# Kernel tuning notes

Measured on AMD Instinct MI355X. Metric: run time of the kernel, lower is better.

The kernel has to match this reference:

```python
import jax, jax.numpy as jnp
import numpy as np

H = 768       # hidden size
NH = 12       # num attention heads
DH = H // NH  # head dim = 64
B = 32
S = 512


def setup_inputs() -> dict:
    key = jax.random.key(0)
    ks = jax.random.split(key, 7)
    scale = 1.0 / np.sqrt(H)
    return {
        "inputs": jax.random.normal(ks[0], (B, S, H), dtype=jnp.float32),
        "Wq": jax.random.normal(ks[1], (H, H), dtype=jnp.float32) * scale,
        "bq": jnp.zeros((H,), dtype=jnp.float32),
        "Wk": jax.random.normal(ks[2], (H, H), dtype=jnp.float32) * scale,
        "bk": jnp.zeros((H,), dtype=jnp.float32),
        "Wv": jax.random.normal(ks[3], (H, H), dtype=jnp.float32) * scale,
        "bv": jnp.zeros((H,), dtype=jnp.float32),
    }


def reference(inputs, Wq, bq, Wk, bk, Wv, bv):
    # BertSelfAttention: linear projections (torch Linear: x @ W.T + b)
    def split_heads(x):  # [B,S,H] -> [B,NH,S,DH]
        return x.reshape(B, S, NH, DH).transpose(0, 2, 1, 3)

    q = split_heads(inputs @ Wq.T + bq)
    k = split_heads(inputs @ Wk.T + bk)
    v = split_heads(inputs @ Wv.T + bv)

    # scores [B,NH,S,S]; the wrapper adds an all-zero attention mask (no-op)
    scores = jnp.einsum("bhqd,bhkd->bhqk", q, k) / jnp.sqrt(jnp.float32(DH))
    probs = jax.nn.softmax(scores, axis=-1)
    ctx = jnp.einsum("bhqk,bhkd->bhqd", probs, v)  # [B,NH,S,DH]
    ctx = ctx.transpose(0, 2, 1, 3).reshape(B, S, H)
    return jnp.tanh(ctx)
```

## Files before the change

kernel.cpp:

```cpp
#include <hip/hip_runtime.h>
#include <hip/hip_bf16.h>
#include <cmath>

#define Bc   32
#define Sc_  512
#define Hc   768
#define NHc  12
#define DHc  64
#define Mc   (Bc * Sc_)
#define Ntot (3 * Hc)

#define QSCALE 0.18033688011112042f

typedef __attribute__((ext_vector_type(8))) short short8v;
typedef __attribute__((ext_vector_type(8))) unsigned short ushort8v;
typedef __attribute__((ext_vector_type(4))) float f32x4;

static __device__ __forceinline__ ushort f2b(float f) {
    __hip_bfloat16 h = __float2bfloat16(f);
    return *reinterpret_cast<ushort*>(&h);
}
static __device__ __forceinline__ ushort2 f2b2(float a, float b) {
    __hip_bfloat162 h = __float22bfloat162_rn(float2{a, b});
    return *reinterpret_cast<ushort2*>(&h);
}

static __device__ __forceinline__ void gl2lds(const ushort* g, ushort* l) {
    __builtin_amdgcn_global_load_lds(
        (const __attribute__((address_space(1))) unsigned int*)g,
        (__attribute__((address_space(3))) unsigned int*)l, 16, 0, 0);
}

static __device__ __forceinline__ float fast_tanh(float x) {
    float e = __builtin_amdgcn_exp2f(x * 2.885390081777927f);
    return 1.0f - 2.0f * __builtin_amdgcn_rcpf(e + 1.0f);
}

__global__ __launch_bounds__(256) void convert_pack(
    const float* __restrict__ X,
    const float* __restrict__ Wq, const float* __restrict__ Wk,
    const float* __restrict__ Wv,
    const float* __restrict__ bq, const float* __restrict__ bk,
    const float* __restrict__ bv,
    ushort* __restrict__ Xt, ushort* __restrict__ Wt, float* __restrict__ bbp)
{
    const int bx = blockIdx.x;
    const int panel = bx / 12, kcg = bx % 12;
    const int t = threadIdx.x;

    __shared__ ushort T[128][68];

    const float* base;
    ushort* out;
    if (panel < 128) {
        base = X + (size_t)panel * 128 * Hc;
        out  = Xt + (size_t)panel * (96 * 1024);
    } else {
        int nblk = panel - 128;
        int n0 = nblk * 128;
        int z = n0 / Hc;
        int nn0 = n0 - z * Hc;
        const float* W = (z == 0) ? Wq : (z == 1) ? Wk : Wv;
        base = W + (size_t)nn0 * Hc;
        out  = Wt + (size_t)nblk * (96 * 1024);
    }
    const int k0 = kcg * 64;

    const int slot = t & 15, rsub = t >> 4;
    #pragma unroll
    for (int rnd = 0; rnd < 8; ++rnd) {
        int row = rnd * 16 + rsub;
        const float* p = base + (size_t)row * Hc + k0 + slot * 4;
        float4 f = *(const float4*)p;
        ushort2 h0 = f2b2(f.x, f.y);
        ushort2 h1 = f2b2(f.z, f.w);
        ushort4 u;
        u.x = h0.x; u.y = h0.y; u.z = h1.x; u.w = h1.y;
        *(ushort4*)&T[row][slot * 4] = u;
    }
    __syncthreads();

    const int row_w = t & 127, kh = t >> 7;
    #pragma unroll
    for (int rnd = 0; rnd < 4; ++rnd) {
        int kc_l = rnd * 2 + kh;
        ushort4 lo = *(const ushort4*)&T[row_w][kc_l * 8];
        ushort4 hi = *(const ushort4*)&T[row_w][kc_l * 8 + 4];
        ushort8v o;
        o[0] = lo.x; o[1] = lo.y; o[2] = lo.z; o[3] = lo.w;
        o[4] = hi.x; o[5] = hi.y; o[6] = hi.z; o[7] = hi.w;
        *(ushort8v*)&out[(size_t)(kcg * 8 + kc_l) * 1024 + row_w * 8] = o;
    }

    if (bx == 0) {
        for (int i = t; i < Ntot; i += 256) {
            int z = i / Hc, nn = i - z * Hc;
            bbp[i] = ((z == 0) ? bq : (z == 1) ? bk : bv)[nn];
        }
    }
}

__global__ __launch_bounds__(256) void qkv_mfma(
    const ushort* __restrict__ Xt, const ushort* __restrict__ Wt,
    const float* __restrict__ bbp,
    ushort* __restrict__ Qb, ushort* __restrict__ Kt, ushort* __restrict__ Vt)
{
    const int tid = threadIdx.x;
    const int wave = tid >> 6, lane = tid & 63;
    const int quad = lane >> 4, l16 = lane & 15;
    const int wr = wave >> 1, wc = wave & 1;
    const int m0 = blockIdx.x * 128;
    const int n0 = blockIdx.y * 128;

    __shared__ __align__(16) ushort As[4096];
    __shared__ __align__(16) ushort Bs[4096];

    f32x4 acc[4][4];
    #pragma unroll
    for (int i = 0; i < 4; ++i)
        #pragma unroll
        for (int j = 0; j < 4; ++j) acc[i][j] = (f32x4)(0.f);

    const ushort* gA = Xt + (size_t)blockIdx.x * (96 * 1024) + wave * 1024 + lane * 8;
    const ushort* gB = Wt + (size_t)blockIdx.y * (96 * 1024) + wave * 1024 + lane * 8;
    ushort* lA = As + wave * 1024;
    ushort* lB = Bs + wave * 1024;

    for (int t = 0; t < 24; ++t) {
        const ushort* ga = gA + t * 4096;
        const ushort* gb = gB + t * 4096;
        gl2lds(ga,       lA);
        gl2lds(ga + 512, lA + 512);
        gl2lds(gb,       lB);
        gl2lds(gb + 512, lB + 512);
        __syncthreads();

        short8v a[4], b[4];
        #pragma unroll
        for (int i = 0; i < 4; ++i)
            a[i] = *(const short8v*)&As[quad * 1024 + (wr * 64 + i * 16 + l16) * 8];
        #pragma unroll
        for (int j = 0; j < 4; ++j)
            b[j] = *(const short8v*)&Bs[quad * 1024 + (wc * 64 + j * 16 + l16) * 8];
        #pragma unroll
        for (int i = 0; i < 4; ++i)
            #pragma unroll
            for (int j = 0; j < 4; ++j)
                acc[i][j] = __builtin_amdgcn_mfma_f32_16x16x32_bf16(
                    a[i], b[j], acc[i][j], 0, 0, 0);
        __syncthreads();
    }

    const int z = n0 / Hc;
    #pragma unroll
    for (int j = 0; j < 4; ++j) {
        const int n  = n0 + wc * 64 + j * 16 + l16;
        const int nn = n - z * Hc;
        const int h  = nn >> 6, d = nn & 63;
        const float bias = bbp[n];
        #pragma unroll
        for (int i = 0; i < 4; ++i) {
            const int mbase = m0 + wr * 64 + i * 16 + quad * 4;
            const int bb = mbase >> 9;
            const int s0 = mbase & 511;
            const size_t head = (size_t)(bb * NHc + h) * (Sc_ * DHc);
            if (z == 0) {
                size_t base = head + (size_t)s0 * DHc + d;
                #pragma unroll
                for (int r = 0; r < 4; ++r)
                    Qb[base + (size_t)r * DHc] = f2b((acc[i][j][r] + bias) * QSCALE);
            } else if (z == 1) {
                size_t base = head + (s0 >> 6) * 4096 + (d >> 3) * 512
                            + (s0 & 63) * 8 + (d & 7);
                #pragma unroll
                for (int r = 0; r < 4; ++r)
                    Kt[base + r * 8] = f2b(acc[i][j][r] + bias);
            } else {
                size_t base = head + (s0 >> 6) * 4096 + ((s0 & 63) >> 3) * 512
                            + d * 8 + (s0 & 7);
                ushort4 o;
                o.x = f2b(acc[i][j][0] + bias);
                o.y = f2b(acc[i][j][1] + bias);
                o.z = f2b(acc[i][j][2] + bias);
                o.w = f2b(acc[i][j][3] + bias);
                *(ushort4*)&Vt[base] = o;
            }
        }
    }
}

__global__ __launch_bounds__(256) void attn_mfma(
    const ushort* __restrict__ Qb, const ushort* __restrict__ Kt,
    const ushort* __restrict__ Vt, float* __restrict__ out)
{
    const int bid = blockIdx.x;
    const int super = bid >> 5, l = bid & 31;
    const int head_lin = super * 8 + (l & 7);
    const int qt = l >> 3;
    const int b = head_lin / NHc, h = head_lin % NHc;

    const int wave = threadIdx.x >> 6;
    const int lane = threadIdx.x & 63;
    const int quad = lane >> 4, l16 = lane & 15;
    const int q0 = qt * 128 + wave * 32;
    const int sw = l16 & 7;

    const size_t head = (size_t)head_lin * (Sc_ * DHc);
    const ushort* __restrict__ Q = Qb + head;
    const ushort* __restrict__ K = Kt + head;
    const ushort* __restrict__ V = Vt + head;

    __shared__ __align__(16) ushort Plds[4][2][1024];

    short8v aq[2][2];
    #pragma unroll
    for (int u = 0; u < 2; ++u)
        #pragma unroll
        for (int hf = 0; hf < 2; ++hf)
            aq[u][hf] = *(const short8v*)
                &Q[(size_t)(q0 + u * 16 + l16) * DHc + hf * 32 + quad * 8];

    short8v ones;
    #pragma unroll
    for (int i = 0; i < 8; ++i) ones[i] = (short)0x3F80;

    f32x4 o[2][4], rsum[2];
    #pragma unroll
    for (int u = 0; u < 2; ++u) {
        rsum[u] = (f32x4)(0.f);
        #pragma unroll
        for (int t = 0; t < 4; ++t) o[u][t] = (f32x4)(0.f);
    }

    #pragma unroll 2
    for (int kb = 0; kb < 8; ++kb) {
        const ushort* Kb_ = K + kb * 4096;
        const ushort* Vb_ = V + kb * 4096;

        short8v kf[4][2], vf[4][2];
        #pragma unroll
        for (int t = 0; t < 4; ++t) {
            kf[t][0] = *(const short8v*)&Kb_[quad * 512 + (t * 16 + l16) * 8];
            kf[t][1] = *(const short8v*)&Kb_[(4 + quad) * 512 + (t * 16 + l16) * 8];
            vf[t][0] = *(const short8v*)&Vb_[quad * 512 + (t * 16 + l16) * 8];
            vf[t][1] = *(const short8v*)&Vb_[(4 + quad) * 512 + (t * 16 + l16) * 8];
        }

        f32x4 sa[2][4];
        #pragma unroll
        for (int u = 0; u < 2; ++u)
            #pragma unroll
            for (int t = 0; t < 4; ++t) {
                f32x4 s = __builtin_amdgcn_mfma_f32_16x16x32_bf16(
                    kf[t][0], aq[u][0], (f32x4)(0.f), 0, 0, 0);
                sa[u][t] = __builtin_amdgcn_mfma_f32_16x16x32_bf16(
                    kf[t][1], aq[u][1], s, 0, 0, 0);
            }

        #pragma unroll
        for (int u = 0; u < 2; ++u) {
            #pragma unroll
            for (int t = 0; t < 4; ++t) {
                float p0 = __builtin_amdgcn_exp2f(sa[u][t][0]);
                float p1 = __builtin_amdgcn_exp2f(sa[u][t][1]);
                float p2 = __builtin_amdgcn_exp2f(sa[u][t][2]);
                float p3 = __builtin_amdgcn_exp2f(sa[u][t][3]);
                ushort2 lo = f2b2(p0, p1);
                ushort2 hi = f2b2(p2, p3);
                ushort4 pk;
                pk.x = lo.x; pk.y = lo.y; pk.z = hi.x; pk.w = hi.y;
                int c = t * 2 + (quad >> 1);
                int addr = l16 * 64 + ((c ^ sw) * 8) + (quad & 1) * 4;
                *(ushort4*)&Plds[wave][u][addr] = pk;
            }
        }

        short8v pa[2][2];
        #pragma unroll
        for (int u = 0; u < 2; ++u) {
            pa[u][0] = *(const short8v*)&Plds[wave][u][l16 * 64 + ((quad ^ sw) * 8)];
            pa[u][1] = *(const short8v*)&Plds[wave][u][l16 * 64 + (((4 + quad) ^ sw) * 8)];
        }

        #pragma unroll
        for (int u = 0; u < 2; ++u) {
            rsum[u] = __builtin_amdgcn_mfma_f32_16x16x32_bf16(
                pa[u][0], ones, rsum[u], 0, 0, 0);
            rsum[u] = __builtin_amdgcn_mfma_f32_16x16x32_bf16(
                pa[u][1], ones, rsum[u], 0, 0, 0);
        }

        #pragma unroll
        for (int t2 = 0; t2 < 4; ++t2)
            #pragma unroll
            for (int u = 0; u < 2; ++u) {
                o[u][t2] = __builtin_amdgcn_mfma_f32_16x16x32_bf16(
                    pa[u][0], vf[t2][0], o[u][t2], 0, 0, 0);
                o[u][t2] = __builtin_amdgcn_mfma_f32_16x16x32_bf16(
                    pa[u][1], vf[t2][1], o[u][t2], 0, 0, 0);
            }
    }

    #pragma unroll
    for (int u = 0; u < 2; ++u) {
        #pragma unroll
        for (int r = 0; r < 4; ++r) {
            float inv = __builtin_amdgcn_rcpf(rsum[u][r]);
            int q = q0 + u * 16 + quad * 4 + r;
            size_t base = ((size_t)b * Sc_ + q) * Hc + h * DHc;
            #pragma unroll
            for (int t2 = 0; t2 < 4; ++t2)
                out[base + t2 * 16 + l16] = fast_tanh(o[u][t2][r] * inv);
        }
    }
}

extern "C" void kernel_launch(void* const* d_in, const int* in_sizes, int n_in,
                              void* d_out, int out_size, void* d_ws, size_t ws_size,
                              hipStream_t stream) {
    const float* X  = (const float*)d_in[0];
    const float* Wq = (const float*)d_in[1];
    const float* bq = (const float*)d_in[2];
    const float* Wk = (const float*)d_in[3];
    const float* bk = (const float*)d_in[4];
    const float* Wv = (const float*)d_in[5];
    const float* bv = (const float*)d_in[6];
    float* out = (float*)d_out;

    ushort* Qb  = (ushort*)d_ws;
    ushort* Kt  = Qb + (size_t)Mc * Hc;
    ushort* Vt  = Kt + (size_t)Mc * Hc;
    ushort* Xt  = Vt + (size_t)Mc * Hc;
    ushort* Wt  = Xt + (size_t)Mc * Hc;
    float*  bbp = (float*)(Wt + (size_t)Ntot * Hc);

    convert_pack<<<dim3(1752), 256, 0, stream>>>(
        X, Wq, Wk, Wv, bq, bk, bv, Xt, Wt, bbp);

    dim3 g1(Mc / 128, Ntot / 128);
    qkv_mfma<<<g1, 256, 0, stream>>>(Xt, Wt, bbp, Qb, Kt, Vt);

    attn_mfma<<<dim3(1536), 256, 0, stream>>>(Qb, Kt, Vt, out);
}
```

Baseline: 235.7 us.

## Fuse fp32-to-bf16 conversion of X into the QKV GEMM A-tile load

The QKV GEMM now reads fp32 inputs straight from global memory, converts them to bf16 in registers and writes them into the LDS A-tile. The separate pre-pass that converted and packed X is removed, so only the weights are still packed. This drops a full read of X and a write plus re-read of a bf16 copy, and cuts one large launch. In exchange, each GEMM block loads twice as many bytes of A across its many column blocks, and those loads go through registers synchronously instead of the asynchronous global-to-LDS path. The unroll pragma on the attention key-block loop is also removed.

```diff
diff --git a/kernel.cpp b/kernel.cpp
--- a/kernel.cpp
+++ b/kernel.cpp
@@ -36,34 +36,25 @@
     return 1.0f - 2.0f * __builtin_amdgcn_rcpf(e + 1.0f);
 }
 
-__global__ __launch_bounds__(256) void convert_pack(
-    const float* __restrict__ X,
+__global__ __launch_bounds__(256) void pack_w(
     const float* __restrict__ Wq, const float* __restrict__ Wk,
     const float* __restrict__ Wv,
     const float* __restrict__ bq, const float* __restrict__ bk,
     const float* __restrict__ bv,
-    ushort* __restrict__ Xt, ushort* __restrict__ Wt, float* __restrict__ bbp)
+    ushort* __restrict__ Wt, float* __restrict__ bbp)
 {
     const int bx = blockIdx.x;
-    const int panel = bx / 12, kcg = bx % 12;
+    const int nblk = bx / 12, kcg = bx % 12;
     const int t = threadIdx.x;
 
     __shared__ ushort T[128][68];
 
-    const float* base;
-    ushort* out;
-    if (panel < 128) {
-        base = X + (size_t)panel * 128 * Hc;
-        out  = Xt + (size_t)panel * (96 * 1024);
-    } else {
-        int nblk = panel - 128;
-        int n0 = nblk * 128;
-        int z = n0 / Hc;
-        int nn0 = n0 - z * Hc;
-        const float* W = (z == 0) ? Wq : (z == 1) ? Wk : Wv;
-        base = W + (size_t)nn0 * Hc;
-        out  = Wt + (size_t)nblk * (96 * 1024);
-    }
+    const int n0 = nblk * 128;
+    const int z = n0 / Hc;
+    const int nn0 = n0 - z * Hc;
+    const float* W = (z == 0) ? Wq : (z == 1) ? Wk : Wv;
+    const float* base = W + (size_t)nn0 * Hc;
+    ushort* out = Wt + (size_t)nblk * (96 * 1024);
     const int k0 = kcg * 64;
 
     const int slot = t & 15, rsub = t >> 4;
@@ -94,14 +85,14 @@
 
     if (bx == 0) {
         for (int i = t; i < Ntot; i += 256) {
-            int z = i / Hc, nn = i - z * Hc;
-            bbp[i] = ((z == 0) ? bq : (z == 1) ? bk : bv)[nn];
+            int z2 = i / Hc, nn = i - z2 * Hc;
+            bbp[i] = ((z2 == 0) ? bq : (z2 == 1) ? bk : bv)[nn];
         }
     }
 }
 
 __global__ __launch_bounds__(256) void qkv_mfma(
-    const ushort* __restrict__ Xt, const ushort* __restrict__ Wt,
+    const float* __restrict__ X, const ushort* __restrict__ Wt,
     const float* __restrict__ bbp,
     ushort* __restrict__ Qb, ushort* __restrict__ Kt, ushort* __restrict__ Vt)
 {
@@ -121,18 +112,38 @@
         #pragma unroll
         for (int j = 0; j < 4; ++j) acc[i][j] = (f32x4)(0.f);
 
-    const ushort* gA = Xt + (size_t)blockIdx.x * (96 * 1024) + wave * 1024 + lane * 8;
+    const int kcA = tid & 3;
+    const int rowA = tid >> 2;
+    const float* Xp = X + (size_t)m0 * Hc;
+
     const ushort* gB = Wt + (size_t)blockIdx.y * (96 * 1024) + wave * 1024 + lane * 8;
-    ushort* lA = As + wave * 1024;
     ushort* lB = Bs + wave * 1024;
 
     for (int t = 0; t < 24; ++t) {
-        const ushort* ga = gA + t * 4096;
         const ushort* gb = gB + t * 4096;
-        gl2lds(ga,       lA);
-        gl2lds(ga + 512, lA + 512);
         gl2lds(gb,       lB);
         gl2lds(gb + 512, lB + 512);
+
+        {
+            const float* xp0 = Xp + (size_t)rowA * Hc + t * 32 + kcA * 8;
+            const float* xp1 = xp0 + (size_t)64 * Hc;
+            float4 f0 = *(const float4*)&xp0[0];
+            float4 f1 = *(const float4*)&xp0[4];
+            float4 f2 = *(const float4*)&xp1[0];
+            float4 f3 = *(const float4*)&xp1[4];
+            ushort2 a0 = f2b2(f0.x, f0.y), a1 = f2b2(f0.z, f0.w);
+            ushort2 a2 = f2b2(f1.x, f1.y), a3 = f2b2(f1.z, f1.w);
+            ushort8v u0;
+            u0[0] = a0.x; u0[1] = a0.y; u0[2] = a1.x; u0[3] = a1.y;
+            u0[4] = a2.x; u0[5] = a2.y; u0[6] = a3.x; u0[7] = a3.y;
+            *(ushort8v*)&As[(kcA * 128 + rowA) * 8] = u0;
+            ushort2 b0 = f2b2(f2.x, f2.y), b1 = f2b2(f2.z, f2.w);
+            ushort2 b2 = f2b2(f3.x, f3.y), b3 = f2b2(f3.z, f3.w);
+            ushort8v u1;
+            u1[0] = b0.x; u1[1] = b0.y; u1[2] = b1.x; u1[3] = b1.y;
+            u1[4] = b2.x; u1[5] = b2.y; u1[6] = b3.x; u1[7] = b3.y;
+            *(ushort8v*)&As[(kcA * 128 + rowA + 64) * 8] = u1;
+        }
         __syncthreads();
 
         short8v a[4], b[4];
@@ -232,7 +243,6 @@
         for (int t = 0; t < 4; ++t) o[u][t] = (f32x4)(0.f);
     }
 
-    #pragma unroll 2
     for (int kb = 0; kb < 8; ++kb) {
         const ushort* Kb_ = K + kb * 4096;
         const ushort* Vb_ = V + kb * 4096;
@@ -330,15 +340,13 @@
     ushort* Qb  = (ushort*)d_ws;
     ushort* Kt  = Qb + (size_t)Mc * Hc;
     ushort* Vt  = Kt + (size_t)Mc * Hc;
-    ushort* Xt  = Vt + (size_t)Mc * Hc;
-    ushort* Wt  = Xt + (size_t)Mc * Hc;
+    ushort* Wt  = Vt + (size_t)Mc * Hc;
     float*  bbp = (float*)(Wt + (size_t)Ntot * Hc);
 
-    convert_pack<<<dim3(1752), 256, 0, stream>>>(
-        X, Wq, Wk, Wv, bq, bk, bv, Xt, Wt, bbp);
+    pack_w<<<dim3(216), 256, 0, stream>>>(Wq, Wk, Wv, bq, bk, bv, Wt, bbp);
 
     dim3 g1(Mc / 128, Ntot / 128);
-    qkv_mfma<<<g1, 256, 0, stream>>>(Xt, Wt, bbp, Qb, Kt, Vt);
+    qkv_mfma<<<g1, 256, 0, stream>>>(X, Wt, bbp, Qb, Kt, Vt);
 
     attn_mfma<<<dim3(1536), 256, 0, stream>>>(Qb, Kt, Vt, out);
 }
```

Result: slower. 258.7 us (+9.8%).

## Double attention query rows per wave to halve K/V fragment reloads

Applied to the files above, without the earlier changes.

Each wave in the attention kernel now handles 64 query rows instead of 32, so every block covers 256 queries and the grid shrinks from 1536 to 768 blocks. Each K/V fragment loaded from global memory is reused across four query sub-tiles rather than two, halving K/V traffic per query. The P staging buffer in LDS is reused per sub-tile, which makes the score, softmax and PV steps run serially inside the u loop, and the kb loop unroll pragma is removed. The trade-offs are higher accumulator register pressure (with launch bounds asking for 2 blocks), fewer blocks to spread across CUs, and less instruction-level overlap.

```diff
diff --git a/kernel.cpp b/kernel.cpp
--- a/kernel.cpp
+++ b/kernel.cpp
@@ -94,8 +94,8 @@
 
     if (bx == 0) {
         for (int i = t; i < Ntot; i += 256) {
-            int z = i / Hc, nn = i - z * Hc;
-            bbp[i] = ((z == 0) ? bq : (z == 1) ? bk : bv)[nn];
+            int z2 = i / Hc, nn = i - z2 * Hc;
+            bbp[i] = ((z2 == 0) ? bq : (z2 == 1) ? bk : bv)[nn];
         }
     }
 }
@@ -189,20 +189,20 @@
     }
 }
 
-__global__ __launch_bounds__(256) void attn_mfma(
+__global__ __launch_bounds__(256, 2) void attn_mfma(
     const ushort* __restrict__ Qb, const ushort* __restrict__ Kt,
     const ushort* __restrict__ Vt, float* __restrict__ out)
 {
     const int bid = blockIdx.x;
-    const int super = bid >> 5, l = bid & 31;
+    const int super = bid >> 4, l = bid & 15;
     const int head_lin = super * 8 + (l & 7);
-    const int qt = l >> 3;
+    const int qhalf = l >> 3;
     const int b = head_lin / NHc, h = head_lin % NHc;
 
     const int wave = threadIdx.x >> 6;
     const int lane = threadIdx.x & 63;
     const int quad = lane >> 4, l16 = lane & 15;
-    const int q0 = qt * 128 + wave * 32;
+    const int q0 = qhalf * 256 + wave * 64;
     const int sw = l16 & 7;
 
     const size_t head = (size_t)head_lin * (Sc_ * DHc);
@@ -210,11 +210,11 @@
     const ushort* __restrict__ K = Kt + head;
     const ushort* __restrict__ V = Vt + head;
 
-    __shared__ __align__(16) ushort Plds[4][2][1024];
-
-    short8v aq[2][2];
-    #pragma unroll
-    for (int u = 0; u < 2; ++u)
+    __shared__ __align__(16) ushort Plds[4][1024];
+
+    short8v aq[4][2];
+    #pragma unroll
+    for (int u = 0; u < 4; ++u)
         #pragma unroll
         for (int hf = 0; hf < 2; ++hf)
             aq[u][hf] = *(const short8v*)
@@ -224,15 +224,14 @@
     #pragma unroll
     for (int i = 0; i < 8; ++i) ones[i] = (short)0x3F80;
 
-    f32x4 o[2][4], rsum[2];
-    #pragma unroll
-    for (int u = 0; u < 2; ++u) {
+    f32x4 o[4][4], rsum[4];
+    #pragma unroll
+    for (int u = 0; u < 4; ++u) {
         rsum[u] = (f32x4)(0.f);
         #pragma unroll
         for (int t = 0; t < 4; ++t) o[u][t] = (f32x4)(0.f);
     }
 
-    #pragma unroll 2
     for (int kb = 0; kb < 8; ++kb) {
         const ushort* Kb_ = K + kb * 4096;
         const ushort* Vb_ = V + kb * 4096;
@@ -246,63 +245,52 @@
             vf[t][1] = *(const short8v*)&Vb_[(4 + quad) * 512 + (t * 16 + l16) * 8];
         }
 
-        f32x4 sa[2][4];
-        #pragma unroll
-        for (int u = 0; u < 2; ++u)
+        #pragma unroll
+        for (int u = 0; u < 4; ++u) {
+            f32x4 sa[4];
             #pragma unroll
             for (int t = 0; t < 4; ++t) {
                 f32x4 s = __builtin_amdgcn_mfma_f32_16x16x32_bf16(
                     kf[t][0], aq[u][0], (f32x4)(0.f), 0, 0, 0);
-                sa[u][t] = __builtin_amdgcn_mfma_f32_16x16x32_bf16(
+                sa[t] = __builtin_amdgcn_mfma_f32_16x16x32_bf16(
                     kf[t][1], aq[u][1], s, 0, 0, 0);
             }
 
-        #pragma unroll
-        for (int u = 0; u < 2; ++u) {
             #pragma unroll
             for (int t = 0; t < 4; ++t) {
-                float p0 = __builtin_amdgcn_exp2f(sa[u][t][0]);
-                float p1 = __builtin_amdgcn_exp2f(sa[u][t][1]);
-                float p2 = __builtin_amdgcn_exp2f(sa[u][t][2]);
-                float p3 = __builtin_amdgcn_exp2f(sa[u][t][3]);
+                float p0 = __builtin_amdgcn_exp2f(sa[t][0]);
+                float p1 = __builtin_amdgcn_exp2f(sa[t][1]);
+                float p2 = __builtin_amdgcn_exp2f(sa[t][2]);
+                float p3 = __builtin_amdgcn_exp2f(sa[t][3]);
                 ushort2 lo = f2b2(p0, p1);
                 ushort2 hi = f2b2(p2, p3);
                 ushort4 pk;
                 pk.x = lo.x; pk.y = lo.y; pk.z = hi.x; pk.w = hi.y;
                 int c = t * 2 + (quad >> 1);
                 int addr = l16 * 64 + ((c ^ sw) * 8) + (quad & 1) * 4;
-                *(ushort4*)&Plds[wave][u][addr] = pk;
+                *(ushort4*)&Plds[wave][addr] = pk;
             }
-        }
-
-        short8v pa[2][2];
-        #pragma unroll
-        for (int u = 0; u < 2; ++u) {
-            pa[u][0] = *(const short8v*)&Plds[wave][u][l16 * 64 + ((quad ^ sw) * 8)];
-            pa[u][1] = *(const short8v*)&Plds[wave][u][l16 * 64 + (((4 + quad) ^ sw) * 8)];
-        }
-
-        #pragma unroll
-        for (int u = 0; u < 2; ++u) {
+
+            short8v pa0 = *(const short8v*)&Plds[wave][l16 * 64 + ((quad ^ sw) * 8)];
+            short8v pa1 = *(const short8v*)&Plds[wave][l16 * 64 + (((4 + quad) ^ sw) * 8)];
+
             rsum[u] = __builtin_amdgcn_mfma_f32_16x16x32_bf16(
-                pa[u][0], ones, rsum[u], 0, 0, 0);
+                pa0, ones, rsum[u], 0, 0, 0);
             rsum[u] = __builtin_amdgcn_mfma_f32_16x16x32_bf16(
-                pa[u][1], ones, rsum[u], 0, 0, 0);
-        }
-
-        #pragma unroll
-        for (int t2 = 0; t2 < 4; ++t2)
-            #pragma unroll
-            for (int u = 0; u < 2; ++u) {
+                pa1, ones, rsum[u], 0, 0, 0);
+
+            #pragma unroll
+            for (int t2 = 0; t2 < 4; ++t2) {
                 o[u][t2] = __builtin_amdgcn_mfma_f32_16x16x32_bf16(
-                    pa[u][0], vf[t2][0], o[u][t2], 0, 0, 0);
+                    pa0, vf[t2][0], o[u][t2], 0, 0, 0);
                 o[u][t2] = __builtin_amdgcn_mfma_f32_16x16x32_bf16(
-                    pa[u][1], vf[t2][1], o[u][t2], 0, 0, 0);
+                    pa1, vf[t2][1], o[u][t2], 0, 0, 0);
             }
-    }
-
-    #pragma unroll
-    for (int u = 0; u < 2; ++u) {
+        }
+    }
+
+    #pragma unroll
+    for (int u = 0; u < 4; ++u) {
         #pragma unroll
         for (int r = 0; r < 4; ++r) {
             float inv = __builtin_amdgcn_rcpf(rsum[u][r]);
@@ -340,5 +328,5 @@
     dim3 g1(Mc / 128, Ntot / 128);
     qkv_mfma<<<g1, 256, 0, stream>>>(Xt, Wt, bbp, Qb, Kt, Vt);
 
-    attn_mfma<<<dim3(1536), 256, 0, stream>>>(Qb, Kt, Vt, out);
-}
+    attn_mfma<<<dim3(768), 256, 0, stream>>>(Qb, Kt, Vt, out);
+}
```

Result: faster. 222.9 us (-5.4%).
